# Performance work log

Measured on AMD Instinct MI355X. Metric: run time of the kernel, lower is better.

Reference implementation:

```python
import jax, jax.numpy as jnp
import numpy as np

N = 50000   # nodes (single node type)
E = 200000  # edges per relation
R = 2       # relations (etypes)
D = 256     # in_dim == out_dim
H = 8       # heads
DK = D // H # 32
SQRT_DK = float(np.sqrt(DK))


def setup_inputs() -> dict:
    key = jax.random.key(0)
    ks = jax.random.split(key, 12)
    wsc = 1.0 / np.sqrt(D)   # linear-layer scale
    rsc = 1.0 / np.sqrt(DK)  # xavier-ish scale for relation tensors
    return {
        "x": jax.random.normal(ks[0], (N, D), jnp.float32),
        "src": jax.random.randint(ks[1], (R, E), 0, N, jnp.int32),
        "dst": jax.random.randint(ks[2], (R, E), 0, N, jnp.int32),
        "Wk": jax.random.normal(ks[3], (D, D), jnp.float32) * wsc,
        "bk": jnp.zeros((D,), jnp.float32),
        "Wq": jax.random.normal(ks[4], (D, D), jnp.float32) * wsc,
        "bq": jnp.zeros((D,), jnp.float32),
        "Wv": jax.random.normal(ks[5], (D, D), jnp.float32) * wsc,
        "bv": jnp.zeros((D,), jnp.float32),
        "Wa": jax.random.normal(ks[6], (D, D), jnp.float32) * wsc,
        "ba": jnp.zeros((D,), jnp.float32),
        "rel_pri": jnp.ones((R, H), jnp.float32),
        "rel_att": jax.random.normal(ks[7], (R, H, DK, DK), jnp.float32) * rsc,
        "rel_msg": jax.random.normal(ks[8], (R, H, DK, DK), jnp.float32) * rsc,
        "skip": jnp.ones((1,), jnp.float32),
    }


def reference(x, src, dst, Wk, bk, Wq, bq, Wv, bv, Wa, ba, rel_pri, rel_att, rel_msg, skip):
    # Per-type K/Q/V projections (single node type) -> [N,H,DK]
    k = (x @ Wk + bk).reshape(N, H, DK)
    q = (x @ Wq + bq).reshape(N, H, DK)
    v = (x @ Wv + bv).reshape(N, H, DK)

    # edge_attention: per-relation bmm transform of gathered src features
    key_t = jnp.einsum('rehd,rhdf->rehf', k[src], rel_att)   # [R,E,H,DK]
    val = jnp.einsum('rehd,rhdf->rehf', v[src], rel_msg)     # [R,E,H,DK]
    att = (q[dst] * key_t).sum(-1) * rel_pri[:, None, :] / SQRT_DK  # [R,E,H]

    # segment softmax over incoming edges per (relation, dst node)
    seg = (dst + N * jnp.arange(R, dtype=dst.dtype)[:, None]).reshape(-1)  # [R*E]
    att_f = att.reshape(R * E, H)
    m = jax.ops.segment_max(att_f, seg, num_segments=R * N)
    m = jnp.where(jnp.isfinite(m), m, 0.0)  # empty segments -> never gathered
    e = jnp.exp(att_f - m[seg])
    den = jax.ops.segment_sum(e, seg, num_segments=R * N)
    attn = e / den[seg]                                       # [R*E,H]

    # weighted-sum scatter aggregation, then cross_reducer='mean' over relations
    h = jax.ops.segment_sum(attn[:, :, None] * val.reshape(R * E, H, DK), seg,
                            num_segments=R * N)               # [R*N,H,DK]
    t = h.reshape(R, N, D).mean(axis=0)                        # [N,D]

    # skip-gated output projection (dropout inactive in eval, use_norm=False)
    alpha = jax.nn.sigmoid(skip[0])
    return (t @ Wa + ba) * alpha + x * (1.0 - alpha)
```

## Files before the change

### kernel.cpp

```cpp
#include <hip/hip_runtime.h>
#include <hip/hip_bf16.h>
#include <math.h>

#define NN 50000
#define EE 200000
#define DD 256
#define HH 8
#define DKK 32
#define NSEG (2 * NN)
#define SCAN_BLOCKS ((NSEG + 1023) / 1024)
#define MPAD 50048
#define LDQKV 1280

constexpr float RSQRT_DK = 0.17677669529663687f;

__device__ __forceinline__ float bf_lo(unsigned u) { return __uint_as_float(u << 16); }
__device__ __forceinline__ float bf_hi(unsigned u) { return __uint_as_float(u & 0xffff0000u); }
__device__ __forceinline__ unsigned short f2bf(float f) {
    unsigned u = __float_as_uint(f);
    return (unsigned short)((u + 0x7fffu + ((u >> 16) & 1u)) >> 16);
}

typedef __attribute__((ext_vector_type(8))) short bf16x8;
typedef __attribute__((ext_vector_type(4))) float f32x4;

#define GLDS16(g, l)                                                                   \
    __builtin_amdgcn_global_load_lds((const __attribute__((address_space(1))) unsigned int*)(g), \
                                     (__attribute__((address_space(3))) unsigned int*)(l), 16, 0, 0)

__global__ void cast_x_kernel(const float* __restrict__ x, unsigned short* __restrict__ xb) {
    const size_t i = ((size_t)blockIdx.x * 256 + threadIdx.x) * 4;
    float4 v = *(const float4*)&x[i];
    ushort4 o;
    o.x = f2bf(v.x); o.y = f2bf(v.y); o.z = f2bf(v.z); o.w = f2bf(v.w);
    *(ushort4*)&xb[i] = o;
}

__global__ void fold_qkv_kernel(const float* __restrict__ Wq, const float* __restrict__ Wk,
                                const float* __restrict__ Wv, const float* __restrict__ bq,
                                const float* __restrict__ bk, const float* __restrict__ bv,
                                const float* __restrict__ rel_att, const float* __restrict__ rel_msg,
                                const float* __restrict__ Wa, unsigned short* __restrict__ wa_t,
                                unsigned short* __restrict__ Wt, float* __restrict__ bb) {
    const int n = blockIdx.x, kk = threadIdx.x;
    if (n >= 1280) {
        const int nn = n - 1280;
        wa_t[(size_t)nn * 256 + kk] = f2bf(Wa[(size_t)kk * 256 + nn]);
        return;
    }
    if (n < 256) {
        Wt[(size_t)n * 256 + kk] = f2bf(Wq[(size_t)kk * 256 + n]);
        if (kk == 0) bb[n] = bq[n];
        return;
    }
    const int sec = (n - 256) >> 8;
    const int c = (n - 256) & 255;
    const int h = c >> 5, f = c & 31;
    const float* W    = (sec < 2) ? Wk : Wv;
    const float* bsrc = (sec < 2) ? bk : bv;
    const float* T = ((sec < 2) ? rel_att : rel_msg)
                   + (size_t)(sec & 1) * HH * DKK * DKK + (size_t)h * DKK * DKK + f;
    const float* wrow = &W[(size_t)kk * 256 + h * 32];
    float s = 0.f;
    #pragma unroll
    for (int d = 0; d < 32; ++d) s += wrow[d] * T[(size_t)d * 32];
    Wt[(size_t)n * 256 + kk] = f2bf(s);
    if (kk == 0) {
        float sb = 0.f;
        for (int d = 0; d < 32; ++d) sb += bsrc[h * 32 + d] * T[(size_t)d * 32];
        bb[n] = sb;
    }
}

__global__ __launch_bounds__(256) void mfma_gemm(
        const unsigned short* __restrict__ A, const unsigned short* __restrict__ Bt,
        const float* __restrict__ bias,
        unsigned short* __restrict__ Cbf, float* __restrict__ Cf,
        int M, int ldc, const float* __restrict__ xres, const float* __restrict__ skip) {
    __shared__ __align__(16) unsigned short As[3][8][64][8];
    __shared__ __align__(16) unsigned short Bs[3][8][64][8];
    const int t = threadIdx.x;
    const int w = t >> 6, l = t & 63;

    const int nwg = gridDim.x * gridDim.y;
    int lin = blockIdx.y * gridDim.x + blockIdx.x;
    {
        const int xcd = lin & 7, pos = lin >> 3;
        const int q = nwg >> 3, r = nwg & 7;
        lin = (xcd < r ? xcd * (q + 1) : r * (q + 1) + (xcd - r) * q) + pos;
    }
    const int n0 = (lin % gridDim.x) * 128;
    const int m0 = (lin / gridDim.x) * 128;
    const int wm = w & 1, wn = w >> 1;

    const int sr = l & 15, sq = l >> 4;
    const unsigned short* ga0 = A  + (size_t)(m0 + w * 16 + sr) * 256 + sq * 8;
    const unsigned short* ga1 = A  + (size_t)(m0 + (w + 4) * 16 + sr) * 256 + sq * 8;
    const unsigned short* gb0 = Bt + (size_t)(n0 + w * 16 + sr) * 256 + sq * 8;
    const unsigned short* gb1 = Bt + (size_t)(n0 + (w + 4) * 16 + sr) * 256 + sq * 8;

#define STAGE(buf, k0) do {                    \
        GLDS16(ga0 + (k0), &As[buf][w][0][0]); \
        GLDS16(ga1 + (k0), &As[buf][w + 4][0][0]); \
        GLDS16(gb0 + (k0), &Bs[buf][w][0][0]); \
        GLDS16(gb1 + (k0), &Bs[buf][w + 4][0][0]); } while (0)

    f32x4 acc[4][4];
    #pragma unroll
    for (int mi = 0; mi < 4; ++mi)
        #pragma unroll
        for (int ni = 0; ni < 4; ++ni) acc[mi][ni] = (f32x4){0.f, 0.f, 0.f, 0.f};

    STAGE(0, 0);
    STAGE(1, 32);
    #pragma unroll
    for (int it = 0; it < 8; ++it) {
        if (it < 7) { asm volatile("s_waitcnt vmcnt(4)" ::: "memory"); }
        else        { asm volatile("s_waitcnt vmcnt(0)" ::: "memory"); }
        __builtin_amdgcn_s_barrier();
        __builtin_amdgcn_sched_barrier(0);
        if (it < 6) {
            STAGE((it + 2) % 3, (it + 2) * 32);
        }
        const int b = it % 3;
        bf16x8 af[4], bfr[4];
        #pragma unroll
        for (int i = 0; i < 4; ++i) {
            af[i]  = *(const bf16x8*)&As[b][wm * 4 + i][l][0];
            bfr[i] = *(const bf16x8*)&Bs[b][wn * 4 + i][l][0];
        }
        #pragma unroll
        for (int mi = 0; mi < 4; ++mi)
            #pragma unroll
            for (int ni = 0; ni < 4; ++ni)
                acc[mi][ni] = __builtin_amdgcn_mfma_f32_16x16x32_bf16(af[mi], bfr[ni],
                                                                      acc[mi][ni], 0, 0, 0);
    }
    __syncthreads();

    unsigned short* ep = (w < 2) ? &As[0][0][0][0] : &Bs[0][0][0][0];
    ep += (w & 1) * 4096;
    const int q4 = l >> 4, c15 = l & 15;

    if (Cf == nullptr) {
        #pragma unroll
        for (int ni = 0; ni < 4; ++ni) {
            const float bcol = bias[n0 + wn * 64 + ni * 16 + c15];
            const int g = ni * 2 + (c15 >> 3);
            #pragma unroll
            for (int mi = 0; mi < 4; ++mi)
                #pragma unroll
                for (int p = 0; p < 4; ++p) {
                    const int row = mi * 16 + q4 * 4 + p;
                    ep[row * 64 + ((g ^ (row & 7)) << 3) + (c15 & 7)] =
                        f2bf(acc[mi][ni][p] + bcol);
                }
        }
        __syncthreads();
        const int rs = l >> 3, cc = l & 7;
        #pragma unroll
        for (int i = 0; i < 8; ++i) {
            const int rl = i * 8 + rs;
            const int row = m0 + wm * 64 + rl;
            if (row < M) {
                uint4 v = *(const uint4*)&ep[rl * 64 + ((cc ^ (rl & 7)) << 3)];
                *(uint4*)&Cbf[(size_t)row * (size_t)ldc + n0 + wn * 64 + cc * 8] = v;
            }
        }
    } else {
        const float alpha = 1.f / (1.f + __expf(-skip[0]));
        const float beta = 1.f - alpha;
        float* epf = (float*)ep;
        #pragma unroll
        for (int half = 0; half < 2; ++half) {
            __syncthreads();
            #pragma unroll
            for (int mi2 = 0; mi2 < 2; ++mi2) {
                const int mi = half * 2 + mi2;
                #pragma unroll
                for (int ni = 0; ni < 4; ++ni) {
                    const float bcol = bias[n0 + wn * 64 + ni * 16 + c15];
                    const int g = ni * 4 + (c15 >> 2);
                    #pragma unroll
                    for (int p = 0; p < 4; ++p) {
                        const int row = mi2 * 16 + q4 * 4 + p;
                        epf[row * 64 + ((g ^ (row & 7)) << 2) + (c15 & 3)] =
                            acc[mi][ni][p] + bcol;
                    }
                }
            }
            __syncthreads();
            const int cc = l & 15, rs = l >> 4;
            #pragma unroll
            for (int i = 0; i < 8; ++i) {
                const int rl = i * 4 + rs;
                const int row = m0 + wm * 64 + half * 32 + rl;
                if (row < M) {
                    const int col = n0 + wn * 64 + cc * 4;
                    float4 v = *(const float4*)&epf[rl * 64 + ((cc ^ (rl & 7)) << 2)];
                    float4 xr = *(const float4*)&xres[(size_t)row * 256 + col];
                    v.x = v.x * alpha + xr.x * beta;
                    v.y = v.y * alpha + xr.y * beta;
                    v.z = v.z * alpha + xr.z * beta;
                    v.w = v.w * alpha + xr.w * beta;
                    *(float4*)&Cf[(size_t)row * 256 + col] = v;
                }
            }
        }
    }
#undef STAGE
}

__global__ void count_kernel(const int* __restrict__ dst, int* __restrict__ cnt) {
    int e = blockIdx.x * 256 + threadIdx.x;
    if (e < 2 * EE) atomicAdd(&cnt[(e / EE) * NN + dst[e]], 1);
}

__global__ __launch_bounds__(1024) void scan_local_kernel(const int* __restrict__ cnt,
                                                          int* __restrict__ rowptr,
                                                          int* __restrict__ bsum) {
    __shared__ int sh[1024];
    const int t = threadIdx.x;
    const int idx = blockIdx.x * 1024 + t;
    const int c = (idx < NSEG) ? cnt[idx] : 0;
    sh[t] = c;
    __syncthreads();
    #pragma unroll
    for (int ofs = 1; ofs < 1024; ofs <<= 1) {
        int v = (t >= ofs) ? sh[t - ofs] : 0;
        __syncthreads();
        sh[t] += v;
        __syncthreads();
    }
    if (idx < NSEG) rowptr[idx] = sh[t] - c;
    if (t == 1023) bsum[blockIdx.x] = sh[1023];
}

__global__ void scan_bsum_kernel(int* __restrict__ bsum, int* __restrict__ rowptr) {
    __shared__ int sh[128];
    const int t = threadIdx.x;
    const int v = (t < SCAN_BLOCKS) ? bsum[t] : 0;
    sh[t] = v;
    __syncthreads();
    #pragma unroll
    for (int ofs = 1; ofs < 128; ofs <<= 1) {
        int u = (t >= ofs) ? sh[t - ofs] : 0;
        __syncthreads();
        sh[t] += u;
        __syncthreads();
    }
    if (t < SCAN_BLOCKS) bsum[t] = sh[t] - v;
    if (t == 127) rowptr[NSEG] = sh[127];
}

__global__ __launch_bounds__(1024) void scan_add_kernel(int* __restrict__ rowptr,
                                                        const int* __restrict__ bsum,
                                                        int* __restrict__ cursor) {
    const int idx = blockIdx.x * 1024 + threadIdx.x;
    if (idx < NSEG) {
        const int v = rowptr[idx] + bsum[blockIdx.x];
        rowptr[idx] = v;
        cursor[idx] = v;
    }
}

__global__ void scatter_kernel(const int* __restrict__ src, const int* __restrict__ dst,
                               int* __restrict__ cursor, int* __restrict__ csr_src) {
    int e = blockIdx.x * 256 + threadIdx.x;
    if (e >= 2 * EE) return;
    int seg = (e / EE) * NN + dst[e];
    int pos = atomicAdd(&cursor[seg], 1);
    csr_src[pos] = src[e];
}

__global__ __launch_bounds__(512) void node_agg_kernel(
        const unsigned short* __restrict__ qkv,
        const int* __restrict__ csr_src,
        const int* __restrict__ rowptr,
        const float* __restrict__ pri,
        unsigned short* __restrict__ tt_bf) {
    __shared__ float sh[4][256];
    const int w = threadIdx.x >> 6, lane = threadIdx.x & 63;
    const int nl = w >> 1, r = w & 1;
    const int n = blockIdx.x * 4 + nl;
    const int lh = lane & 31;
    const int eh = lane >> 5;
    const int h = lh >> 2;
    const size_t coff = (size_t)lh * 8;

    const uint4 qv = *(const uint4*)&qkv[(size_t)n * LDQKV + coff];
    const float q0 = bf_lo(qv.x), q1 = bf_hi(qv.x), q2 = bf_lo(qv.y), q3 = bf_hi(qv.y);
    const float q4_ = bf_lo(qv.z), q5 = bf_hi(qv.z), q6 = bf_lo(qv.w), q7 = bf_hi(qv.w);

    const float prm = pri[r * HH + h] * RSQRT_DK;
    const int seg = r * NN + n;
    const int j0 = rowptr[seg], j1 = rowptr[seg + 1];
    const size_t kbase = 256 + (size_t)r * 256 + coff;
    const size_t vbase = 768 + (size_t)r * 256 + coff;

    float a0 = 0.f, a1 = 0.f, a2 = 0.f, a3 = 0.f, a4 = 0.f, a5 = 0.f, a6 = 0.f, a7 = 0.f;
    float den = 0.f;

    int j = j0 + eh;
    uint4 kv, vv;
    bool valid = j < j1;
    if (valid) {
        const size_t rowb = (size_t)csr_src[j] * LDQKV;
        kv = *(const uint4*)&qkv[rowb + kbase];
        vv = *(const uint4*)&qkv[rowb + vbase];
    }
    while (valid) {
        const int jn = j + 2;
        const bool validn = jn < j1;
        uint4 kvn, vvn;
        if (validn) {
            const size_t rowb = (size_t)csr_src[jn] * LDQKV;
            kvn = *(const uint4*)&qkv[rowb + kbase];
            vvn = *(const uint4*)&qkv[rowb + vbase];
        }
        float p = q0 * bf_lo(kv.x) + q1 * bf_hi(kv.x) + q2 * bf_lo(kv.y) + q3 * bf_hi(kv.y)
                + q4_ * bf_lo(kv.z) + q5 * bf_hi(kv.z) + q6 * bf_lo(kv.w) + q7 * bf_hi(kv.w);
        p += __shfl_xor(p, 1);
        p += __shfl_xor(p, 2);
        const float a = __expf(p * prm);
        den += a;
        a0 += a * bf_lo(vv.x); a1 += a * bf_hi(vv.x);
        a2 += a * bf_lo(vv.y); a3 += a * bf_hi(vv.y);
        a4 += a * bf_lo(vv.z); a5 += a * bf_hi(vv.z);
        a6 += a * bf_lo(vv.w); a7 += a * bf_hi(vv.w);
        kv = kvn; vv = vvn; j = jn; valid = validn;
    }
    den += __shfl_xor(den, 32);
    a0 += __shfl_xor(a0, 32); a1 += __shfl_xor(a1, 32);
    a2 += __shfl_xor(a2, 32); a3 += __shfl_xor(a3, 32);
    a4 += __shfl_xor(a4, 32); a5 += __shfl_xor(a5, 32);
    a6 += __shfl_xor(a6, 32); a7 += __shfl_xor(a7, 32);
    const float wgt = (den > 0.f) ? 0.5f / den : 0.f;

    if (r == 0 && eh == 0) {
        sh[nl][0 * 32 + lh] = a0 * wgt; sh[nl][1 * 32 + lh] = a1 * wgt;
        sh[nl][2 * 32 + lh] = a2 * wgt; sh[nl][3 * 32 + lh] = a3 * wgt;
        sh[nl][4 * 32 + lh] = a4 * wgt; sh[nl][5 * 32 + lh] = a5 * wgt;
        sh[nl][6 * 32 + lh] = a6 * wgt; sh[nl][7 * 32 + lh] = a7 * wgt;
    }
    __syncthreads();
    if (r == 1 && eh == 0) {
        const float t0 = sh[nl][0 * 32 + lh] + a0 * wgt;
        const float t1 = sh[nl][1 * 32 + lh] + a1 * wgt;
        const float t2 = sh[nl][2 * 32 + lh] + a2 * wgt;
        const float t3 = sh[nl][3 * 32 + lh] + a3 * wgt;
        const float t4 = sh[nl][4 * 32 + lh] + a4 * wgt;
        const float t5 = sh[nl][5 * 32 + lh] + a5 * wgt;
        const float t6 = sh[nl][6 * 32 + lh] + a6 * wgt;
        const float t7 = sh[nl][7 * 32 + lh] + a7 * wgt;
        uint4 o;
        o.x = (unsigned)f2bf(t0) | ((unsigned)f2bf(t1) << 16);
        o.y = (unsigned)f2bf(t2) | ((unsigned)f2bf(t3) << 16);
        o.z = (unsigned)f2bf(t4) | ((unsigned)f2bf(t5) << 16);
        o.w = (unsigned)f2bf(t6) | ((unsigned)f2bf(t7) << 16);
        *(uint4*)&tt_bf[(size_t)n * 256 + coff] = o;
    }
}

extern "C" void kernel_launch(void* const* d_in, const int* in_sizes, int n_in,
                              void* d_out, int out_size, void* d_ws, size_t ws_size,
                              hipStream_t stream) {
    const float* x       = (const float*)d_in[0];
    const int*   src     = (const int*)d_in[1];
    const int*   dst     = (const int*)d_in[2];
    const float* Wk      = (const float*)d_in[3];
    const float* bk      = (const float*)d_in[4];
    const float* Wq      = (const float*)d_in[5];
    const float* bq      = (const float*)d_in[6];
    const float* Wv      = (const float*)d_in[7];
    const float* bv      = (const float*)d_in[8];
    const float* Wa      = (const float*)d_in[9];
    const float* ba      = (const float*)d_in[10];
    const float* rel_pri = (const float*)d_in[11];
    const float* rel_att = (const float*)d_in[12];
    const float* rel_msg = (const float*)d_in[13];
    const float* skip    = (const float*)d_in[14];
    float* out = (float*)d_out;
    char* ws = (char*)d_ws;

    const size_t ND = (size_t)NN * DD;
    size_t off = 0;
    unsigned short* x_bf   = (unsigned short*)(ws + off); off += (size_t)MPAD * DD * 2;
    unsigned short* qkv_bf = (unsigned short*)(ws + off); off += (size_t)NN * LDQKV * 2;
    unsigned short* tt_bf  = (unsigned short*)(ws + off); off += (size_t)MPAD * DD * 2;
    unsigned short* wqkv_t = (unsigned short*)(ws + off); off += (size_t)LDQKV * 256 * 2;
    unsigned short* wa_t   = (unsigned short*)(ws + off); off += (size_t)256 * 256 * 2;
    float*          bb     = (float*)(ws + off);          off += LDQKV * 4;
    int*            cnt    = (int*)(ws + off);            off += (size_t)NSEG * 4;
    int*            rowptr = (int*)(ws + off);            off += (size_t)(NSEG + 1) * 4;
    int*            cursor = (int*)(ws + off);            off += (size_t)NSEG * 4;
    int*            bsum   = (int*)(ws + off);            off += 128 * 4;
    int*            csr_src= (int*)(ws + off);            off += (size_t)2 * EE * 4;
    if (ws_size < off) return;

    cast_x_kernel<<<(int)(ND / 1024), 256, 0, stream>>>(x, x_bf);
    fold_qkv_kernel<<<1536, 256, 0, stream>>>(Wq, Wk, Wv, bq, bk, bv,
                                              rel_att, rel_msg, Wa, wa_t, wqkv_t, bb);

    dim3 g_qkv(LDQKV / 128, MPAD / 128);
    mfma_gemm<<<g_qkv, 256, 0, stream>>>(x_bf, wqkv_t, bb, qkv_bf, nullptr,
                                         NN, LDQKV, nullptr, nullptr);

    hipMemsetAsync(cnt, 0, (size_t)NSEG * 4, stream);
    const int eg = (2 * EE + 255) / 256;
    count_kernel<<<eg, 256, 0, stream>>>(dst, cnt);
    scan_local_kernel<<<SCAN_BLOCKS, 1024, 0, stream>>>(cnt, rowptr, bsum);
    scan_bsum_kernel<<<1, 128, 0, stream>>>(bsum, rowptr);
    scan_add_kernel<<<SCAN_BLOCKS, 1024, 0, stream>>>(rowptr, bsum, cursor);
    scatter_kernel<<<eg, 256, 0, stream>>>(src, dst, cursor, csr_src);

    node_agg_kernel<<<NN / 4, 512, 0, stream>>>(qkv_bf, csr_src, rowptr,
                                                rel_pri, tt_bf);

    dim3 g_out(DD / 128, MPAD / 128);
    mfma_gemm<<<g_out, 256, 0, stream>>>(tt_bf, wa_t, ba, nullptr, out,
                                         NN, DD, x, skip);
}
```

Baseline: 374.2 us.

## Make GEMM blocks loop over all N tiles with continuous cross-tile prefetch

The 2D grid GEMM becomes a 1D grid where each block owns a 128-row M strip and iterates over every N tile. The three-stage global-to-LDS pipeline runs continuously across N tiles, so loads for the next tile overlap the current tile's MFMAs and epilogue. A separate per-wave epilogue LDS buffer lets the epilogue run without block-wide syncs. The aim is to cut per-tile prologue and barrier overhead and to reuse the A strip through cache. In exchange the grid shrinks to about 391 blocks, which lowers parallelism on the narrow output GEMM, and LDS use per block grows.

```diff
diff --git a/kernel.cpp b/kernel.cpp
--- a/kernel.cpp
+++ b/kernel.cpp
@@ -76,134 +76,142 @@
         const unsigned short* __restrict__ A, const unsigned short* __restrict__ Bt,
         const float* __restrict__ bias,
         unsigned short* __restrict__ Cbf, float* __restrict__ Cf,
-        int M, int ldc, const float* __restrict__ xres, const float* __restrict__ skip) {
+        int M, int N, int ldc, const float* __restrict__ xres, const float* __restrict__ skip) {
     __shared__ __align__(16) unsigned short As[3][8][64][8];
     __shared__ __align__(16) unsigned short Bs[3][8][64][8];
+    __shared__ __align__(16) unsigned short Ep[4][2048];
     const int t = threadIdx.x;
     const int w = t >> 6, l = t & 63;
 
-    const int nwg = gridDim.x * gridDim.y;
-    int lin = blockIdx.y * gridDim.x + blockIdx.x;
+    const int nwg = gridDim.x;
+    int lin = blockIdx.x;
     {
         const int xcd = lin & 7, pos = lin >> 3;
         const int q = nwg >> 3, r = nwg & 7;
         lin = (xcd < r ? xcd * (q + 1) : r * (q + 1) + (xcd - r) * q) + pos;
     }
-    const int n0 = (lin % gridDim.x) * 128;
-    const int m0 = (lin / gridDim.x) * 128;
+    const int m0 = lin * 128;
     const int wm = w & 1, wn = w >> 1;
+    const int NT = N >> 7;
+    const int TS = NT * 8;
 
     const int sr = l & 15, sq = l >> 4;
     const unsigned short* ga0 = A  + (size_t)(m0 + w * 16 + sr) * 256 + sq * 8;
     const unsigned short* ga1 = A  + (size_t)(m0 + (w + 4) * 16 + sr) * 256 + sq * 8;
-    const unsigned short* gb0 = Bt + (size_t)(n0 + w * 16 + sr) * 256 + sq * 8;
-    const unsigned short* gb1 = Bt + (size_t)(n0 + (w + 4) * 16 + sr) * 256 + sq * 8;
-
-#define STAGE(buf, k0) do {                    \
-        GLDS16(ga0 + (k0), &As[buf][w][0][0]); \
-        GLDS16(ga1 + (k0), &As[buf][w + 4][0][0]); \
-        GLDS16(gb0 + (k0), &Bs[buf][w][0][0]); \
-        GLDS16(gb1 + (k0), &Bs[buf][w + 4][0][0]); } while (0)
-
-    f32x4 acc[4][4];
-    #pragma unroll
-    for (int mi = 0; mi < 4; ++mi)
-        #pragma unroll
-        for (int ni = 0; ni < 4; ++ni) acc[mi][ni] = (f32x4){0.f, 0.f, 0.f, 0.f};
-
-    STAGE(0, 0);
-    STAGE(1, 32);
-    #pragma unroll
-    for (int it = 0; it < 8; ++it) {
-        if (it < 7) { asm volatile("s_waitcnt vmcnt(4)" ::: "memory"); }
-        else        { asm volatile("s_waitcnt vmcnt(0)" ::: "memory"); }
-        __builtin_amdgcn_s_barrier();
-        __builtin_amdgcn_sched_barrier(0);
-        if (it < 6) {
-            STAGE((it + 2) % 3, (it + 2) * 32);
-        }
-        const int b = it % 3;
-        bf16x8 af[4], bfr[4];
-        #pragma unroll
-        for (int i = 0; i < 4; ++i) {
-            af[i]  = *(const bf16x8*)&As[b][wm * 4 + i][l][0];
-            bfr[i] = *(const bf16x8*)&Bs[b][wn * 4 + i][l][0];
-        }
+    const unsigned short* gb0 = Bt + (size_t)(w * 16 + sr) * 256 + sq * 8;
+    const unsigned short* gb1 = Bt + (size_t)((w + 4) * 16 + sr) * 256 + sq * 8;
+
+#define STAGE(s_) do {                                                     \
+        const int buf_ = (s_) % 3;                                         \
+        const size_t aoff_ = (size_t)((s_) & 7) * 32;                      \
+        const size_t boff_ = (size_t)((s_) >> 3) * (128 * 256) + aoff_;    \
+        GLDS16(ga0 + aoff_, &As[buf_][w][0][0]);                           \
+        GLDS16(ga1 + aoff_, &As[buf_][w + 4][0][0]);                       \
+        GLDS16(gb0 + boff_, &Bs[buf_][w][0][0]);                           \
+        GLDS16(gb1 + boff_, &Bs[buf_][w + 4][0][0]); } while (0)
+
+    STAGE(0);
+    STAGE(1);
+    const int q4 = l >> 4, c15 = l & 15;
+
+    for (int nt = 0; nt < NT; ++nt) {
+        f32x4 acc[4][4];
         #pragma unroll
         for (int mi = 0; mi < 4; ++mi)
             #pragma unroll
-            for (int ni = 0; ni < 4; ++ni)
-                acc[mi][ni] = __builtin_amdgcn_mfma_f32_16x16x32_bf16(af[mi], bfr[ni],
-                                                                      acc[mi][ni], 0, 0, 0);
-    }
-    __syncthreads();
-
-    unsigned short* ep = (w < 2) ? &As[0][0][0][0] : &Bs[0][0][0][0];
-    ep += (w & 1) * 4096;
-    const int q4 = l >> 4, c15 = l & 15;
-
-    if (Cf == nullptr) {
+            for (int ni = 0; ni < 4; ++ni) acc[mi][ni] = (f32x4){0.f, 0.f, 0.f, 0.f};
+
         #pragma unroll
-        for (int ni = 0; ni < 4; ++ni) {
-            const float bcol = bias[n0 + wn * 64 + ni * 16 + c15];
-            const int g = ni * 2 + (c15 >> 3);
+        for (int kc = 0; kc < 8; ++kc) {
+            const int s = (nt << 3) + kc;
+            if (s == TS - 1)            { asm volatile("s_waitcnt vmcnt(0)" ::: "memory"); }
+            else if (nt == 0 || kc >= 2){ asm volatile("s_waitcnt vmcnt(4)" ::: "memory"); }
+            else if (Cbf != nullptr)    { asm volatile("s_waitcnt vmcnt(12)" ::: "memory"); }
+            else                        { asm volatile("s_waitcnt vmcnt(0)" ::: "memory"); }
+            __builtin_amdgcn_s_barrier();
+            __builtin_amdgcn_sched_barrier(0);
+            if (s + 2 < TS) STAGE(s + 2);
+            const int b = s % 3;
+            bf16x8 af[4], bfr[4];
+            #pragma unroll
+            for (int i = 0; i < 4; ++i) {
+                af[i]  = *(const bf16x8*)&As[b][wm * 4 + i][l][0];
+                bfr[i] = *(const bf16x8*)&Bs[b][wn * 4 + i][l][0];
+            }
             #pragma unroll
             for (int mi = 0; mi < 4; ++mi)
                 #pragma unroll
-                for (int p = 0; p < 4; ++p) {
-                    const int row = mi * 16 + q4 * 4 + p;
-                    ep[row * 64 + ((g ^ (row & 7)) << 3) + (c15 & 7)] =
-                        f2bf(acc[mi][ni][p] + bcol);
+                for (int ni = 0; ni < 4; ++ni)
+                    acc[mi][ni] = __builtin_amdgcn_mfma_f32_16x16x32_bf16(af[mi], bfr[ni],
+                                                                          acc[mi][ni], 0, 0, 0);
+        }
+
+        if (Cf == nullptr) {
+            unsigned short* epw = &Ep[w][0];
+            #pragma unroll
+            for (int hp = 0; hp < 2; ++hp) {
+                #pragma unroll
+                for (int mi2 = 0; mi2 < 2; ++mi2) {
+                    const int mi = hp * 2 + mi2;
+                    #pragma unroll
+                    for (int ni = 0; ni < 4; ++ni) {
+                        const float bcol = bias[nt * 128 + wn * 64 + ni * 16 + c15];
+                        const int g = ni * 2 + (c15 >> 3);
+                        #pragma unroll
+                        for (int p = 0; p < 4; ++p) {
+                            const int rl = mi2 * 16 + q4 * 4 + p;
+                            epw[rl * 64 + ((g ^ (rl & 7)) << 3) + (c15 & 7)] =
+                                f2bf(acc[mi][ni][p] + bcol);
+                        }
+                    }
                 }
-        }
-        __syncthreads();
-        const int rs = l >> 3, cc = l & 7;
-        #pragma unroll
-        for (int i = 0; i < 8; ++i) {
-            const int rl = i * 8 + rs;
-            const int row = m0 + wm * 64 + rl;
-            if (row < M) {
-                uint4 v = *(const uint4*)&ep[rl * 64 + ((cc ^ (rl & 7)) << 3)];
-                *(uint4*)&Cbf[(size_t)row * (size_t)ldc + n0 + wn * 64 + cc * 8] = v;
+                asm volatile("s_waitcnt lgkmcnt(0)" ::: "memory");
+                __builtin_amdgcn_sched_barrier(0);
+                const int rs = l >> 3, cc = l & 7;
+                #pragma unroll
+                for (int i = 0; i < 4; ++i) {
+                    const int rl = i * 8 + rs;
+                    const int row = m0 + wm * 64 + hp * 32 + rl;
+                    if (row < M) {
+                        uint4 v = *(const uint4*)&epw[rl * 64 + ((cc ^ (rl & 7)) << 3)];
+                        *(uint4*)&Cbf[(size_t)row * (size_t)ldc + nt * 128 + wn * 64 + cc * 8] = v;
+                    }
+                }
             }
-        }
-    } else {
-        const float alpha = 1.f / (1.f + __expf(-skip[0]));
-        const float beta = 1.f - alpha;
-        float* epf = (float*)ep;
-        #pragma unroll
-        for (int half = 0; half < 2; ++half) {
-            __syncthreads();
+        } else {
+            const float alpha = 1.f / (1.f + __expf(-skip[0]));
+            const float beta = 1.f - alpha;
+            float* epf = (float*)&Ep[w][0];
             #pragma unroll
-            for (int mi2 = 0; mi2 < 2; ++mi2) {
-                const int mi = half * 2 + mi2;
+            for (int qp = 0; qp < 4; ++qp) {
                 #pragma unroll
                 for (int ni = 0; ni < 4; ++ni) {
-                    const float bcol = bias[n0 + wn * 64 + ni * 16 + c15];
+                    const float bcol = bias[nt * 128 + wn * 64 + ni * 16 + c15];
                     const int g = ni * 4 + (c15 >> 2);
                     #pragma unroll
                     for (int p = 0; p < 4; ++p) {
-                        const int row = mi2 * 16 + q4 * 4 + p;
-                        epf[row * 64 + ((g ^ (row & 7)) << 2) + (c15 & 3)] =
-                            acc[mi][ni][p] + bcol;
+                        const int rl = q4 * 4 + p;
+                        epf[rl * 64 + ((g ^ (rl & 3)) << 2) + (c15 & 3)] =
+                            acc[qp][ni][p] + bcol;
                     }
                 }
-            }
-            __syncthreads();
-            const int cc = l & 15, rs = l >> 4;
-            #pragma unroll
-            for (int i = 0; i < 8; ++i) {
-                const int rl = i * 4 + rs;
-                const int row = m0 + wm * 64 + half * 32 + rl;
-                if (row < M) {
-                    const int col = n0 + wn * 64 + cc * 4;
-                    float4 v = *(const float4*)&epf[rl * 64 + ((cc ^ (rl & 7)) << 2)];
-                    float4 xr = *(const float4*)&xres[(size_t)row * 256 + col];
-                    v.x = v.x * alpha + xr.x * beta;
-                    v.y = v.y * alpha + xr.y * beta;
-                    v.z = v.z * alpha + xr.z * beta;
-                    v.w = v.w * alpha + xr.w * beta;
-                    *(float4*)&Cf[(size_t)row * 256 + col] = v;
+                asm volatile("s_waitcnt lgkmcnt(0)" ::: "memory");
+                __builtin_amdgcn_sched_barrier(0);
+                const int cc = l & 15, rs = l >> 4;
+                #pragma unroll
+                for (int i = 0; i < 4; ++i) {
+                    const int rl = i * 4 + rs;
+                    const int row = m0 + wm * 64 + qp * 16 + rl;
+                    if (row < M) {
+                        const int col = nt * 128 + wn * 64 + cc * 4;
+                        float4 v = *(const float4*)&epf[rl * 64 + ((cc ^ (rl & 3)) << 2)];
+                        float4 xr = *(const float4*)&xres[(size_t)row * 256 + col];
+                        v.x = v.x * alpha + xr.x * beta;
+                        v.y = v.y * alpha + xr.y * beta;
+                        v.z = v.z * alpha + xr.z * beta;
+                        v.w = v.w * alpha + xr.w * beta;
+                        *(float4*)&Cf[(size_t)row * 256 + col] = v;
+                    }
                 }
             }
         }
@@ -402,9 +410,8 @@
     fold_qkv_kernel<<<1536, 256, 0, stream>>>(Wq, Wk, Wv, bq, bk, bv,
                                               rel_att, rel_msg, Wa, wa_t, wqkv_t, bb);
 
-    dim3 g_qkv(LDQKV / 128, MPAD / 128);
-    mfma_gemm<<<g_qkv, 256, 0, stream>>>(x_bf, wqkv_t, bb, qkv_bf, nullptr,
-                                         NN, LDQKV, nullptr, nullptr);
+    mfma_gemm<<<MPAD / 128, 256, 0, stream>>>(x_bf, wqkv_t, bb, qkv_bf, nullptr,
+                                              NN, LDQKV, LDQKV, nullptr, nullptr);
 
     hipMemsetAsync(cnt, 0, (size_t)NSEG * 4, stream);
     const int eg = (2 * EE + 255) / 256;
@@ -417,7 +424,6 @@
     node_agg_kernel<<<NN / 4, 512, 0, stream>>>(qkv_bf, csr_src, rowptr,
                                                 rel_pri, tt_bf);
 
-    dim3 g_out(DD / 128, MPAD / 128);
-    mfma_gemm<<<g_out, 256, 0, stream>>>(tt_bf, wa_t, ba, nullptr, out,
-                                         NN, DD, x, skip);
-}
+    mfma_gemm<<<MPAD / 128, 256, 0, stream>>>(tt_bf, wa_t, ba, nullptr, out,
+                                              NN, DD, DD, x, skip);
+}
```

New measurement: 460.2 us. 1.23x slower.
